# Kernel tuning notes

Hardware: AMD Instinct MI355X
Metric: run time of the kernel (lower is better)

## Reference

```python
import jax, jax.numpy as jnp
import numpy as np

A_BITS = 3
W_BITS = 3

def setup_inputs() -> dict:
    key = jax.random.key(0)
    k1, k2 = jax.random.split(key)
    # activations: small nonnegative ints (will be clipped to [0, 2^A_bits-1])
    x = jax.random.randint(k1, (32, 256, 56, 56), 0, 2 ** A_BITS, dtype=jnp.int32)
    # weights: torch.randint(0, 2**W_bits - 1, ...) -> values in [0, 6]
    weight = jax.random.randint(k2, (256, 256, 3, 3), 0, 2 ** W_BITS - 1).astype(jnp.float32)
    return {"x": x, "weight": weight}

def reference(x, weight):
    # quantize: clip activations to [0, 2^A_bits - 1]; truncate weight to int
    xq = jnp.clip(x.astype(jnp.int32), 0, 2 ** A_BITS - 1).astype(jnp.float32)
    wq = weight.astype(jnp.int32).astype(jnp.float32)  # OIHW, nonneg small ints
    # direct conv2d, stride 1, no padding (VALID). Small ints -> exact in fp32.
    out = jax.lax.conv_general_dilated(
        xq, wq,
        window_strides=(1, 1),
        padding="VALID",
        dimension_numbers=("NCHW", "OIHW", "NCHW"),
    )
    return out  # [32, 256, 54, 54]
```

## Files before the change

kernel.cpp:

```cpp
#include <hip/hip_runtime.h>
#include <stdint.h>

typedef int i32x4 __attribute__((ext_vector_type(4)));
typedef float f32x4 __attribute__((ext_vector_type(4)));

#define N_IMG 32
#define C_IN 256
#define H_IN 56
#define W_IN 56
#define K_OUT 256
#define H_OUT 54
#define W_OUT 54
#define HW_OUT 2916
#define M_PIX 93312
#define CHW_OUT 746496

#define BM 384
#define NSTEP 36

#define XT_BYTES ((size_t)N_IMG * H_IN * W_IN * C_IN)
#define WT_BYTES ((size_t)9 * K_OUT * C_IN)

#define BUF_STRIDE 40960
#define BOFF 24576

__global__ __launch_bounds__(256) void xform(const int* __restrict__ x,
                                             const float* __restrict__ w,
                                             unsigned char* __restrict__ xt,
                                             unsigned char* __restrict__ wt) {
    const int bid = blockIdx.x;
    if (bid < N_IMG * H_IN) {
        const int n = bid / H_IN;
        const int h = bid % H_IN;
        const int c = threadIdx.x;
        const int* src = x + ((size_t)((n * C_IN + c) * H_IN + h)) * W_IN;
        unsigned char* dst = xt + ((size_t)(n * H_IN + h) * W_IN) * C_IN + c;
        #pragma unroll
        for (int w0 = 0; w0 < W_IN; w0 += 4) {
            int4 v = *(const int4*)(src + w0);
            int a[4] = {v.x, v.y, v.z, v.w};
            #pragma unroll
            for (int j = 0; j < 4; ++j) {
                int q = a[j] < 0 ? 0 : (a[j] > 7 ? 7 : a[j]);
                dst[(size_t)(w0 + j) * C_IN] = (unsigned char)q;
            }
        }
    } else {
        const int k = bid - N_IMG * H_IN;
        const int c = threadIdx.x;
        const float* src = w + ((size_t)k * C_IN + c) * 9;
        #pragma unroll
        for (int rs = 0; rs < 9; ++rs) {
            int iv = (int)src[rs];
            wt[((size_t)rs * K_OUT + k) * C_IN + c] = (unsigned char)iv;
        }
    }
}

__device__ __forceinline__ void gload_lds16(const void* g, void* l) {
    __builtin_amdgcn_global_load_lds(
        (const __attribute__((address_space(1))) uint32_t*)g,
        (__attribute__((address_space(3))) uint32_t*)l,
        16, 0, 0);
}

__device__ __forceinline__ unsigned lds_off(const void* p) {
    return (unsigned)(unsigned long long)(__attribute__((address_space(3))) const char*)p;
}

#define DSREAD(dst, addr) \
    asm volatile("ds_read_b128 %0, %1" : "=v"(dst) : "v"(addr))

__device__ __forceinline__ int swz4(int row) { return (row ^ (row >> 2)) & 3; }

__global__ __launch_bounds__(512, 2) void conv_mfma(const unsigned char* __restrict__ xt,
                                                    const unsigned char* __restrict__ wt,
                                                    float* __restrict__ out) {
    __shared__ __align__(16) unsigned char lds[3 * BUF_STRIDE];

    const int t512 = threadIdx.x;
    const int l    = t512 & 63;
    const int wid  = t512 >> 6;
    const int wr   = wid >> 1;
    const int wc   = wid & 1;
    const int mb   = blockIdx.x;

    const int slot = t512 & 3;
    const int trow = t512 >> 2;
    const int tb16 = t512 * 16;

    int srcA[3];
    #pragma unroll
    for (int rnd = 0; rnd < 3; ++rnd) {
        const int r   = rnd * 128 + trow;
        const int m   = mb * BM + r;
        const int n   = m / HW_OUT;
        const int rem = m - n * HW_OUT;
        const int oh  = rem / W_OUT;
        const int ow  = rem - oh * W_OUT;
        srcA[rnd] = ((n * H_IN + oh) * W_IN + ow) * 256 + ((slot ^ swz4(r)) << 4);
    }
    int srcB[2];
    #pragma unroll
    for (int rnd = 0; rnd < 2; ++rnd) {
        const int k = rnd * 128 + trow;
        srcB[rnd] = k * 256 + ((slot ^ swz4(k)) << 4);
    }

    const int lrow = l & 15;
    const int g    = l >> 4;
    unsigned aoff[6], boff[8];
    #pragma unroll
    for (int mf = 0; mf < 6; ++mf) {
        const int r = wr * 96 + mf * 16 + lrow;
        aoff[mf] = (unsigned)(r * 64 + ((g ^ swz4(r)) << 4));
    }
    #pragma unroll
    for (int nf = 0; nf < 8; ++nf) {
        const int k = wc * 128 + nf * 16 + lrow;
        boff[nf] = (unsigned)(BOFF + k * 64 + ((g ^ swz4(k)) << 4));
    }

    i32x4 acc[6][8];
    #pragma unroll
    for (int i = 0; i < 6; ++i)
        #pragma unroll
        for (int j = 0; j < 8; ++j)
            acc[i][j] = (i32x4){0, 0, 0, 0};

    const char* xb = (const char*)xt;
    const char* wb = (const char*)wt;
    const unsigned ldsb = lds_off(lds);

    #define STAGE_A3(T, BUFO) do {                                          \
        const int tap_ = (T) >> 2, cq_ = (T) & 3;                           \
        const int r_ = tap_ / 3, s_ = tap_ - r_ * 3;                        \
        const int ast_ = (r_ * W_IN + s_) * 256 + cq_ * 64;                 \
        gload_lds16(xb + srcA[0] + ast_, lds + (BUFO) + tb16);              \
        gload_lds16(xb + srcA[1] + ast_, lds + (BUFO) + 8192 + tb16);       \
        gload_lds16(xb + srcA[2] + ast_, lds + (BUFO) + 16384 + tb16);      \
    } while (0)
    #define STAGE_B2(T, BUFO) do {                                          \
        const int tap_ = (T) >> 2, cq_ = (T) & 3;                           \
        const int bst_ = tap_ * (K_OUT * C_IN) + cq_ * 64;                  \
        gload_lds16(wb + srcB[0] + bst_, lds + (BUFO) + BOFF + tb16);       \
        gload_lds16(wb + srcB[1] + bst_, lds + (BUFO) + BOFF + 8192 + tb16);\
    } while (0)

    STAGE_A3(0, 0);          STAGE_B2(0, 0);
    STAGE_A3(1, BUF_STRIDE); STAGE_B2(1, BUF_STRIDE);
    asm volatile("s_waitcnt vmcnt(5)" ::: "memory");
    __builtin_amdgcn_s_barrier();

    unsigned curO = 0, nxtO = BUF_STRIDE, stgO = 2 * BUF_STRIDE;

    for (int t = 0; t < NSTEP; ++t) {
        int t2 = t + 2; if (t2 >= NSTEP) t2 -= NSTEP;
        const unsigned aB = ldsb + curO;
        i32x4 a[6], bA[4], bB[4];

        #pragma unroll
        for (int mf = 0; mf < 6; ++mf) DSREAD(a[mf], aB + aoff[mf]);
        #pragma unroll
        for (int nf = 0; nf < 4; ++nf) DSREAD(bA[nf], aB + boff[nf]);
        STAGE_A3(t2, stgO);
        __builtin_amdgcn_s_barrier();
        asm volatile("s_waitcnt lgkmcnt(0)" ::: "memory");
        __builtin_amdgcn_sched_barrier(0);
        __builtin_amdgcn_s_setprio(1);
        #pragma unroll
        for (int mf = 0; mf < 6; ++mf)
            #pragma unroll
            for (int nf = 0; nf < 4; ++nf)
                acc[mf][nf] = __builtin_amdgcn_mfma_i32_16x16x64_i8(
                    a[mf], bA[nf], acc[mf][nf], 0, 0, 0);
        __builtin_amdgcn_s_setprio(0);
        __builtin_amdgcn_s_barrier();

        #pragma unroll
        for (int nf = 0; nf < 4; ++nf) DSREAD(bB[nf], aB + boff[nf + 4]);
        STAGE_B2(t2, stgO);
        __builtin_amdgcn_s_barrier();
        asm volatile("s_waitcnt lgkmcnt(0)" ::: "memory");
        __builtin_amdgcn_sched_barrier(0);
        __builtin_amdgcn_s_setprio(1);
        #pragma unroll
        for (int mf = 0; mf < 6; ++mf)
            #pragma unroll
            for (int nf = 0; nf < 4; ++nf)
                acc[mf][nf + 4] = __builtin_amdgcn_mfma_i32_16x16x64_i8(
                    a[mf], bB[nf], acc[mf][nf + 4], 0, 0, 0);
        __builtin_amdgcn_s_setprio(0);
        asm volatile("s_waitcnt vmcnt(5)" ::: "memory");
        __builtin_amdgcn_s_barrier();

        const unsigned tmp = curO; curO = nxtO; nxtO = stgO; stgO = tmp;
    }

    asm volatile("s_waitcnt vmcnt(0)" ::: "memory");

    const int c16 = l & 15;
    const int p4  = (l >> 4) << 2;
    #pragma unroll
    for (int mf = 0; mf < 6; ++mf) {
        const int m   = mb * BM + wr * 96 + mf * 16 + p4;
        const int n   = m / HW_OUT;
        const int rem = m - n * HW_OUT;
        float* ob = out + (size_t)n * CHW_OUT + rem;
        #pragma unroll
        for (int nf = 0; nf < 8; ++nf) {
            const int ch = wc * 128 + nf * 16 + c16;
            f32x4 v;
            #pragma unroll
            for (int j = 0; j < 4; ++j) v[j] = (float)acc[mf][nf][j];
            *(f32x4*)(ob + (size_t)ch * HW_OUT) = v;
        }
    }
    #undef STAGE_A3
    #undef STAGE_B2
}

__global__ __launch_bounds__(256) void conv_naive(const int* __restrict__ x,
                                                  const float* __restrict__ w,
                                                  float* __restrict__ out) {
    int idx = blockIdx.x * 256 + threadIdx.x;
    if (idx >= N_IMG * K_OUT * HW_OUT) return;
    const int wo = idx % W_OUT;
    int tmp = idx / W_OUT;
    const int ho = tmp % H_OUT; tmp /= H_OUT;
    const int k = tmp % K_OUT;
    const int n = tmp / K_OUT;
    float acc = 0.f;
    for (int c = 0; c < C_IN; ++c) {
        const int* xp = x + ((size_t)((n * C_IN + c) * H_IN + ho)) * W_IN + wo;
        const float* wp = w + ((size_t)(k * C_IN + c)) * 9;
        #pragma unroll
        for (int r = 0; r < 3; ++r)
            #pragma unroll
            for (int s = 0; s < 3; ++s) {
                int xv = xp[r * W_IN + s];
                xv = xv < 0 ? 0 : (xv > 7 ? 7 : xv);
                acc += (float)xv * (float)(int)wp[r * 3 + s];
            }
    }
    out[idx] = acc;
}

extern "C" void kernel_launch(void* const* d_in, const int* in_sizes, int n_in,
                              void* d_out, int out_size, void* d_ws, size_t ws_size,
                              hipStream_t stream) {
    const int*   x = (const int*)d_in[0];
    const float* w = (const float*)d_in[1];
    float* out = (float*)d_out;

    const size_t need = XT_BYTES + WT_BYTES;
    if (ws_size >= need) {
        unsigned char* xt = (unsigned char*)d_ws;
        unsigned char* wt = (unsigned char*)((char*)d_ws + XT_BYTES);
        hipLaunchKernelGGL(xform, dim3(N_IMG * H_IN + K_OUT), dim3(256), 0, stream,
                           x, w, xt, wt);
        hipLaunchKernelGGL(conv_mfma, dim3(M_PIX / BM), dim3(512), 0, stream,
                           xt, wt, out);
    } else {
        const int total = N_IMG * K_OUT * HW_OUT;
        hipLaunchKernelGGL(conv_naive, dim3((total + 255) / 256), dim3(256), 0, stream, x, w, out);
    }
}
```

Measured before the change: 102.2 us.

## Stage input halo once in LDS and reuse across all nine conv taps

Instead of re-gathering an im2col A tile from global memory for every tap and channel quarter, each block loads a contiguous halo of input pixel rows (half the channels at a time) into LDS once and indexes it per tap with row offsets. The M tile halves to 192 pixels and warps are rearranged 2x4, with weights triple-buffered per tap across 128 channels. This is meant to cut redundant global traffic for activations, at the cost of a very large LDS footprint that may limit occupancy, more barriers per step, and twice as many blocks each redoing the weight loads.

```diff
diff --git a/kernel.cpp b/kernel.cpp
--- a/kernel.cpp
+++ b/kernel.cpp
@@ -15,14 +15,13 @@
 #define M_PIX 93312
 #define CHW_OUT 746496
 
-#define BM 384
-#define NSTEP 36
+#define BM 192
 
 #define XT_BYTES ((size_t)N_IMG * H_IN * W_IN * C_IN)
 #define WT_BYTES ((size_t)9 * K_OUT * C_IN)
 
-#define BUF_STRIDE 40960
-#define BOFF 24576
+#define HALO_BYTES 57344
+#define B_STRIDE 32768
 
 __global__ __launch_bounds__(256) void xform(const int* __restrict__ x,
                                              const float* __restrict__ w,
@@ -70,134 +69,191 @@
 
 #define DSREAD(dst, addr) \
     asm volatile("ds_read_b128 %0, %1" : "=v"(dst) : "v"(addr))
-
-__device__ __forceinline__ int swz4(int row) { return (row ^ (row >> 2)) & 3; }
+#define BAR __builtin_amdgcn_s_barrier()
+#define LGKM0 do { asm volatile("s_waitcnt lgkmcnt(0)" ::: "memory"); \
+                   __builtin_amdgcn_sched_barrier(0); } while (0)
 
 __global__ __launch_bounds__(512, 2) void conv_mfma(const unsigned char* __restrict__ xt,
                                                     const unsigned char* __restrict__ wt,
                                                     float* __restrict__ out) {
-    __shared__ __align__(16) unsigned char lds[3 * BUF_STRIDE];
+    __shared__ __align__(16) unsigned char lds[155648];
 
     const int t512 = threadIdx.x;
     const int l    = t512 & 63;
     const int wid  = t512 >> 6;
-    const int wr   = wid >> 1;
-    const int wc   = wid & 1;
+    const int wr   = wid >> 2;
+    const int wc   = wid & 3;
     const int mb   = blockIdx.x;
 
-    const int slot = t512 & 3;
-    const int trow = t512 >> 2;
+    const int slot = t512 & 7;
+    const int srow = t512 >> 3;
+    const int cs   = ((slot ^ (srow & 7)) << 4);
     const int tb16 = t512 * 16;
-
-    int srcA[3];
+    const int sb   = srow * 256 + cs;
+
+    const int m0  = mb * BM;
+    const int n0  = m0 / HW_OUT;
+    const int rm0 = m0 - n0 * HW_OUT;
+    const int oh0 = rm0 / W_OUT;
+    const int ow0 = rm0 - oh0 * W_OUT;
+    const int pix0 = n0 * (H_IN * W_IN) + oh0 * W_IN + ow0;
+
+    const int lrow = l & 15;
+    int drow[6];
     #pragma unroll
-    for (int rnd = 0; rnd < 3; ++rnd) {
-        const int r   = rnd * 128 + trow;
-        const int m   = mb * BM + r;
+    for (int mf = 0; mf < 6; ++mf) {
+        const int m   = m0 + wr * 96 + mf * 16 + lrow;
         const int n   = m / HW_OUT;
         const int rem = m - n * HW_OUT;
         const int oh  = rem / W_OUT;
         const int ow  = rem - oh * W_OUT;
-        srcA[rnd] = ((n * H_IN + oh) * W_IN + ow) * 256 + ((slot ^ swz4(r)) << 4);
-    }
-    int srcB[2];
+        drow[mf] = n * (H_IN * W_IN) + oh * W_IN + ow - pix0;
+    }
+
+    const int g16 = (l >> 4) << 4;
+    const unsigned ck[2] = { (unsigned)g16, (unsigned)(64 + g16) };
+    const unsigned swzB = (unsigned)((lrow & 7) << 4);
+    unsigned boffk[4][2];
     #pragma unroll
-    for (int rnd = 0; rnd < 2; ++rnd) {
-        const int k = rnd * 128 + trow;
-        srcB[rnd] = k * 256 + ((slot ^ swz4(k)) << 4);
-    }
-
-    const int lrow = l & 15;
-    const int g    = l >> 4;
-    unsigned aoff[6], boff[8];
-    #pragma unroll
-    for (int mf = 0; mf < 6; ++mf) {
-        const int r = wr * 96 + mf * 16 + lrow;
-        aoff[mf] = (unsigned)(r * 64 + ((g ^ swz4(r)) << 4));
-    }
-    #pragma unroll
-    for (int nf = 0; nf < 8; ++nf) {
-        const int k = wc * 128 + nf * 16 + lrow;
-        boff[nf] = (unsigned)(BOFF + k * 64 + ((g ^ swz4(k)) << 4));
-    }
-
-    i32x4 acc[6][8];
+    for (int nf = 0; nf < 4; ++nf) {
+        const unsigned rb = (unsigned)((wc * 64 + nf * 16 + lrow) << 7);
+        boffk[nf][0] = rb + (ck[0] ^ swzB);
+        boffk[nf][1] = rb + (ck[1] ^ swzB);
+    }
+
+    i32x4 acc[6][4];
     #pragma unroll
     for (int i = 0; i < 6; ++i)
         #pragma unroll
-        for (int j = 0; j < 8; ++j)
+        for (int j = 0; j < 4; ++j)
             acc[i][j] = (i32x4){0, 0, 0, 0};
 
     const char* xb = (const char*)xt;
     const char* wb = (const char*)wt;
     const unsigned ldsb = lds_off(lds);
 
-    #define STAGE_A3(T, BUFO) do {                                          \
-        const int tap_ = (T) >> 2, cq_ = (T) & 3;                           \
-        const int r_ = tap_ / 3, s_ = tap_ - r_ * 3;                        \
-        const int ast_ = (r_ * W_IN + s_) * 256 + cq_ * 64;                 \
-        gload_lds16(xb + srcA[0] + ast_, lds + (BUFO) + tb16);              \
-        gload_lds16(xb + srcA[1] + ast_, lds + (BUFO) + 8192 + tb16);       \
-        gload_lds16(xb + srcA[2] + ast_, lds + (BUFO) + 16384 + tb16);      \
+    #define STAGE_HALO(H) do {                                               \
+        const char* hs_ = xb + (size_t)pix0 * 256 + (H) * 128 + sb;          \
+        _Pragma("unroll")                                                    \
+        for (int i_ = 0; i_ < 7; ++i_)                                       \
+            gload_lds16(hs_ + (size_t)i_ * 16384, lds + i_ * 8192 + tb16);   \
     } while (0)
-    #define STAGE_B2(T, BUFO) do {                                          \
-        const int tap_ = (T) >> 2, cq_ = (T) & 3;                           \
-        const int bst_ = tap_ * (K_OUT * C_IN) + cq_ * 64;                  \
-        gload_lds16(wb + srcB[0] + bst_, lds + (BUFO) + BOFF + tb16);       \
-        gload_lds16(wb + srcB[1] + bst_, lds + (BUFO) + BOFF + 8192 + tb16);\
+
+    #define STAGE_B4(T) do {                                                 \
+        const int h_ = (T) >= 9, tp_ = (T) - (h_ ? 9 : 0);                   \
+        const char* bs_ = wb + tp_ * 65536 + h_ * 128 + sb;                  \
+        unsigned char* bd_ = lds + HALO_BYTES + ((T) % 3) * B_STRIDE + tb16; \
+        _Pragma("unroll")                                                    \
+        for (int p_ = 0; p_ < 4; ++p_)                                       \
+            gload_lds16(bs_ + p_ * 16384, bd_ + p_ * 8192);                  \
     } while (0)
 
-    STAGE_A3(0, 0);          STAGE_B2(0, 0);
-    STAGE_A3(1, BUF_STRIDE); STAGE_B2(1, BUF_STRIDE);
-    asm volatile("s_waitcnt vmcnt(5)" ::: "memory");
-    __builtin_amdgcn_s_barrier();
-
-    unsigned curO = 0, nxtO = BUF_STRIDE, stgO = 2 * BUF_STRIDE;
-
-    for (int t = 0; t < NSTEP; ++t) {
-        int t2 = t + 2; if (t2 >= NSTEP) t2 -= NSTEP;
-        const unsigned aB = ldsb + curO;
-        i32x4 a[6], bA[4], bB[4];
-
-        #pragma unroll
-        for (int mf = 0; mf < 6; ++mf) DSREAD(a[mf], aB + aoff[mf]);
-        #pragma unroll
-        for (int nf = 0; nf < 4; ++nf) DSREAD(bA[nf], aB + boff[nf]);
-        STAGE_A3(t2, stgO);
-        __builtin_amdgcn_s_barrier();
-        asm volatile("s_waitcnt lgkmcnt(0)" ::: "memory");
-        __builtin_amdgcn_sched_barrier(0);
+    STAGE_HALO(0);
+    STAGE_B4(0);
+    STAGE_B4(1);
+    asm volatile("s_waitcnt vmcnt(4)" ::: "memory");
+    BAR;
+
+    unsigned o0 = 0, o1 = B_STRIDE, o2 = 2 * B_STRIDE;
+
+    for (int t = 0; t < 18; ++t) {
+        const int h    = (t >= 9);
+        const int tap  = t - (h ? 9 : 0);
+        const int r    = tap / 3;
+        const int s    = tap - r * 3;
+        const int toff = r * W_IN + s;
+        const int t2   = t + 2;
+        const bool stg = (t2 < 18);
+        const int h2   = (t2 >= 9);
+        const int tap2 = t2 - (h2 ? 9 : 0);
+        const char* bsrc2 = wb + tap2 * 65536 + h2 * 128 + sb;
+        unsigned char* bdst2 = lds + HALO_BYTES + tb16;
+        const unsigned bB = ldsb + HALO_BYTES + o0;
+
+        i32x4 av[3], bv[4];
+
+        #pragma unroll
+        for (int i = 0; i < 3; ++i) {
+            const int row = drow[i] + toff;
+            DSREAD(av[i], ldsb + ((unsigned)row << 7) + (ck[0] ^ ((unsigned)(row & 7) << 4)));
+        }
+        #pragma unroll
+        for (int nf = 0; nf < 4; ++nf) DSREAD(bv[nf], bB + boffk[nf][0]);
+        if (stg) gload_lds16(bsrc2, bdst2 + o2);
+        BAR; LGKM0;
         __builtin_amdgcn_s_setprio(1);
         #pragma unroll
-        for (int mf = 0; mf < 6; ++mf)
+        for (int i = 0; i < 3; ++i)
             #pragma unroll
             for (int nf = 0; nf < 4; ++nf)
-                acc[mf][nf] = __builtin_amdgcn_mfma_i32_16x16x64_i8(
-                    a[mf], bA[nf], acc[mf][nf], 0, 0, 0);
+                acc[i][nf] = __builtin_amdgcn_mfma_i32_16x16x64_i8(av[i], bv[nf], acc[i][nf], 0, 0, 0);
         __builtin_amdgcn_s_setprio(0);
-        __builtin_amdgcn_s_barrier();
-
-        #pragma unroll
-        for (int nf = 0; nf < 4; ++nf) DSREAD(bB[nf], aB + boff[nf + 4]);
-        STAGE_B2(t2, stgO);
-        __builtin_amdgcn_s_barrier();
-        asm volatile("s_waitcnt lgkmcnt(0)" ::: "memory");
-        __builtin_amdgcn_sched_barrier(0);
+        BAR;
+
+        #pragma unroll
+        for (int i = 0; i < 3; ++i) {
+            const int row = drow[3 + i] + toff;
+            DSREAD(av[i], ldsb + ((unsigned)row << 7) + (ck[0] ^ ((unsigned)(row & 7) << 4)));
+        }
+        if (stg) gload_lds16(bsrc2 + 16384, bdst2 + o2 + 8192);
+        BAR; LGKM0;
         __builtin_amdgcn_s_setprio(1);
         #pragma unroll
-        for (int mf = 0; mf < 6; ++mf)
+        for (int i = 0; i < 3; ++i)
             #pragma unroll
             for (int nf = 0; nf < 4; ++nf)
-                acc[mf][nf + 4] = __builtin_amdgcn_mfma_i32_16x16x64_i8(
-                    a[mf], bB[nf], acc[mf][nf + 4], 0, 0, 0);
+                acc[3 + i][nf] = __builtin_amdgcn_mfma_i32_16x16x64_i8(av[i], bv[nf], acc[3 + i][nf], 0, 0, 0);
         __builtin_amdgcn_s_setprio(0);
-        asm volatile("s_waitcnt vmcnt(5)" ::: "memory");
-        __builtin_amdgcn_s_barrier();
-
-        const unsigned tmp = curO; curO = nxtO; nxtO = stgO; stgO = tmp;
-    }
-
-    asm volatile("s_waitcnt vmcnt(0)" ::: "memory");
+        BAR;
+
+        #pragma unroll
+        for (int i = 0; i < 3; ++i) {
+            const int row = drow[i] + toff;
+            DSREAD(av[i], ldsb + ((unsigned)row << 7) + (ck[1] ^ ((unsigned)(row & 7) << 4)));
+        }
+        #pragma unroll
+        for (int nf = 0; nf < 4; ++nf) DSREAD(bv[nf], bB + boffk[nf][1]);
+        if (stg) gload_lds16(bsrc2 + 32768, bdst2 + o2 + 16384);
+        BAR; LGKM0;
+        __builtin_amdgcn_s_setprio(1);
+        #pragma unroll
+        for (int i = 0; i < 3; ++i)
+            #pragma unroll
+            for (int nf = 0; nf < 4; ++nf)
+                acc[i][nf] = __builtin_amdgcn_mfma_i32_16x16x64_i8(av[i], bv[nf], acc[i][nf], 0, 0, 0);
+        __builtin_amdgcn_s_setprio(0);
+        BAR;
+
+        #pragma unroll
+        for (int i = 0; i < 3; ++i) {
+            const int row = drow[3 + i] + toff;
+            DSREAD(av[i], ldsb + ((unsigned)row << 7) + (ck[1] ^ ((unsigned)(row & 7) << 4)));
+        }
+        if (stg) gload_lds16(bsrc2 + 49152, bdst2 + o2 + 24576);
+        BAR; LGKM0;
+        __builtin_amdgcn_s_setprio(1);
+        #pragma unroll
+        for (int i = 0; i < 3; ++i)
+            #pragma unroll
+            for (int nf = 0; nf < 4; ++nf)
+                acc[3 + i][nf] = __builtin_amdgcn_mfma_i32_16x16x64_i8(av[i], bv[nf], acc[3 + i][nf], 0, 0, 0);
+        __builtin_amdgcn_s_setprio(0);
+
+        if (t == 8) {
+            BAR;
+            STAGE_HALO(1);
+            asm volatile("s_waitcnt vmcnt(0)" ::: "memory");
+            BAR;
+        } else if (t == 16) {
+            asm volatile("s_waitcnt vmcnt(0)" ::: "memory");
+            BAR;
+        } else if (t < 16) {
+            asm volatile("s_waitcnt vmcnt(4)" ::: "memory");
+            BAR;
+        }
+
+        const unsigned tmp = o0; o0 = o1; o1 = o2; o2 = tmp;
+    }
 
     const int c16 = l & 15;
     const int p4  = (l >> 4) << 2;
@@ -208,16 +264,16 @@
         const int rem = m - n * HW_OUT;
         float* ob = out + (size_t)n * CHW_OUT + rem;
         #pragma unroll
-        for (int nf = 0; nf < 8; ++nf) {
-            const int ch = wc * 128 + nf * 16 + c16;
+        for (int nf = 0; nf < 4; ++nf) {
+            const int ch = wc * 64 + nf * 16 + c16;
             f32x4 v;
             #pragma unroll
             for (int j = 0; j < 4; ++j) v[j] = (float)acc[mf][nf][j];
             *(f32x4*)(ob + (size_t)ch * HW_OUT) = v;
         }
     }
-    #undef STAGE_A3
-    #undef STAGE_B2
+    #undef STAGE_HALO
+    #undef STAGE_B4
 }
 
 __global__ __launch_bounds__(256) void conv_naive(const int* __restrict__ x,
```

New measurement: 103.8 us. About the same (+1.5%).
